# Optimization experiments

Hardware: AMD Instinct MI355X
Metric: run time of the kernel (lower is better)

Reference implementation:

```python
import jax, jax.numpy as jnp
import numpy as np
import math

N, D, C = 1024, 512, 70722
M_MARGIN = 0.4
H_SCALE = 0.333
S_SCALE = 64.0
EPS = 0.001


def setup_inputs() -> dict:
    key = jax.random.key(0)
    k1, k2, k3 = jax.random.split(key, 3)
    x = jax.random.normal(k1, (N, D), dtype=jnp.float32)
    labels = jax.random.randint(k2, (N,), 0, C, dtype=jnp.int64)
    # weights ~ N(0, 0.01) as in nn.Parameter init
    weights = 0.01 * jax.random.normal(k3, (C, D), dtype=jnp.float32)
    return {"x": x, "labels": labels, "weights": weights}


def reference(x, labels, weights):
    # world_size == 1: all-gather is identity and all labels are local.
    x_norms = jnp.maximum(jnp.linalg.norm(x, axis=1, keepdims=True), 1e-8)  # [N,1]

    norm_emb = x / jnp.maximum(jnp.linalg.norm(x, axis=1, keepdims=True), 1e-12)
    norm_w = weights / jnp.maximum(jnp.linalg.norm(weights, axis=1, keepdims=True), 1e-12)
    cosine = jnp.clip(norm_emb @ norm_w.T, -1.0, 1.0)  # [N,C]

    # AdaFace adaptive margin scaler (detached norms; t_alpha=1 -> batch stats = current stats)
    safe_norms = jax.lax.stop_gradient(jnp.clip(x_norms, 0.001, 100.0))  # [N,1]
    batch_mean = jnp.mean(safe_norms)
    batch_std = jnp.std(safe_norms, ddof=1)  # torch .std() is unbiased
    margin_scaler = jnp.clip((safe_norms - batch_mean) / (batch_std + EPS) * H_SCALE, -1.0, 1.0)  # [N,1]

    g_angular = -M_MARGIN * margin_scaler           # [N,1]
    g_add = M_MARGIN + M_MARGIN * margin_scaler     # [N,1]

    onehot = jax.nn.one_hot(labels, C, dtype=cosine.dtype)  # [N,C]

    theta = jnp.arccos(cosine)
    theta_m = jnp.clip(theta + onehot * g_angular, EPS, math.pi - EPS)
    logits = (jnp.cos(theta_m) - onehot * g_add) * S_SCALE  # [N,C]

    logp = jax.nn.log_softmax(logits, axis=-1)
    loss = -jnp.mean(jnp.take_along_axis(logp, labels[:, None], axis=1))
    return loss
```

## Files before the change

kernel.cpp:

```cpp
#include <hip/hip_runtime.h>
#include <hip/hip_bf16.h>
#include <stdint.h>

#define DIM 512
#define NROWS 1024
#define NCLS 70722
#define NCTILE 553

typedef float floatx4 __attribute__((ext_vector_type(4)));

__device__ __forceinline__ unsigned pk4_fp8(float a, float b, float c, float d) {
    unsigned v = 0;
    v = __builtin_amdgcn_cvt_pk_fp8_f32(a, b, v, false);
    v = __builtin_amdgcn_cvt_pk_fp8_f32(c, d, v, true);
    return v;
}

__device__ __forceinline__ float wave_reduce_sum(float s) {
    #pragma unroll
    for (int m = 1; m < 64; m <<= 1) s += __shfl_xor(s, m);
    return s;
}

__global__ __launch_bounds__(256) void prep_kernel(
        const float* __restrict__ x, const float* __restrict__ W,
        const int* __restrict__ labels,
        uint8_t* __restrict__ An, uint8_t* __restrict__ Wn8,
        float* __restrict__ rownorm, float* __restrict__ coslab,
        float* __restrict__ rowsum) {
    int b = blockIdx.x;
    int wv = threadIdx.x >> 6, lane = threadIdx.x & 63;
    if (b < NROWS / 4) {
        if (threadIdx.x < 4) rowsum[b * 4 + threadIdx.x] = 0.0f;
        int row = b * 4 + wv;
        int lab = labels[row];
        const float4* xs = (const float4*)(x + (size_t)row * DIM);
        const float4* ws = (const float4*)(W + (size_t)lab * DIM);
        float4 xa = xs[lane * 2], xb = xs[lane * 2 + 1];
        float4 wa = ws[lane * 2], wb = ws[lane * 2 + 1];
        float dxx = xa.x*xa.x + xa.y*xa.y + xa.z*xa.z + xa.w*xa.w
                  + xb.x*xb.x + xb.y*xb.y + xb.z*xb.z + xb.w*xb.w;
        float dww = wa.x*wa.x + wa.y*wa.y + wa.z*wa.z + wa.w*wa.w
                  + wb.x*wb.x + wb.y*wb.y + wb.z*wb.z + wb.w*wb.w;
        float dxw = xa.x*wa.x + xa.y*wa.y + xa.z*wa.z + xa.w*wa.w
                  + xb.x*wb.x + xb.y*wb.y + xb.z*wb.z + xb.w*wb.w;
        dxx = wave_reduce_sum(dxx);
        dww = wave_reduce_sum(dww);
        dxw = wave_reduce_sum(dxw);
        float norm = sqrtf(dxx);
        float s16 = 16.0f / fmaxf(norm, 1e-12f);
        uint2 p;
        p.x = pk4_fp8(xa.x*s16, xa.y*s16, xa.z*s16, xa.w*s16);
        p.y = pk4_fp8(xb.x*s16, xb.y*s16, xb.z*s16, xb.w*s16);
        *(uint2*)(An + (size_t)row * DIM + lane * 8) = p;
        if (lane == 0) {
            rownorm[row] = norm;
            coslab[row]  = dxw / (fmaxf(norm, 1e-12f) * fmaxf(sqrtf(dww), 1e-12f));
        }
    } else {
        int c = (b - NROWS / 4) * 16 + wv * 4 + (lane >> 4);
        c = min(c, NCLS - 1);
        int l16 = lane & 15;
        const float4* src = (const float4*)(W + (size_t)c * DIM + l16 * 32);
        float4 v[8];
        #pragma unroll
        for (int i = 0; i < 8; ++i) v[i] = src[i];
        float ss = 0.0f;
        #pragma unroll
        for (int i = 0; i < 8; ++i)
            ss += v[i].x*v[i].x + v[i].y*v[i].y + v[i].z*v[i].z + v[i].w*v[i].w;
        ss += __shfl_xor(ss, 1); ss += __shfl_xor(ss, 2);
        ss += __shfl_xor(ss, 4); ss += __shfl_xor(ss, 8);
        float s16 = 16.0f / fmaxf(sqrtf(ss), 1e-12f);
        uint4 q0, q1;
        q0.x = pk4_fp8(v[0].x*s16, v[0].y*s16, v[0].z*s16, v[0].w*s16);
        q0.y = pk4_fp8(v[1].x*s16, v[1].y*s16, v[1].z*s16, v[1].w*s16);
        q0.z = pk4_fp8(v[2].x*s16, v[2].y*s16, v[2].z*s16, v[2].w*s16);
        q0.w = pk4_fp8(v[3].x*s16, v[3].y*s16, v[3].z*s16, v[3].w*s16);
        q1.x = pk4_fp8(v[4].x*s16, v[4].y*s16, v[4].z*s16, v[4].w*s16);
        q1.y = pk4_fp8(v[5].x*s16, v[5].y*s16, v[5].z*s16, v[5].w*s16);
        q1.z = pk4_fp8(v[6].x*s16, v[6].y*s16, v[6].z*s16, v[6].w*s16);
        q1.w = pk4_fp8(v[7].x*s16, v[7].y*s16, v[7].z*s16, v[7].w*s16);
        uint4* dst = (uint4*)(Wn8 + (size_t)c * DIM + l16 * 32);
        dst[0] = q0;
        dst[1] = q1;
    }
}

__global__ __launch_bounds__(256) void gemm5_kernel(
        const uint8_t* __restrict__ An, const uint8_t* __restrict__ Wn8,
        float* __restrict__ rowsum) {
    __shared__ uint8_t As[128 * 64];
    __shared__ uint8_t Bs[128 * 64];
    __shared__ float red[128];
    int b = blockIdx.x;
    int ctile = (b >> 6) * 8 + (b & 7);
    int mtile = (b >> 3) & 7;
    if (ctile >= NCTILE) return;
    int t = threadIdx.x, lane = t & 63, wv = t >> 6;
    if (t < 128) red[t] = 0.0f;

    int sr = lane >> 2;
    int ck = (((lane & 3) ^ (sr & 3)) * 16);
    const uint8_t* aG = An + (size_t)(mtile * 128 + wv * 16 + sr) * DIM + ck;
    int c0 = min(ctile * 128 + wv * 16 + sr,      NCLS - 1);
    int c1 = min(ctile * 128 + 64 + wv * 16 + sr, NCLS - 1);
    const uint8_t* bG0 = Wn8 + (size_t)c0 * DIM + ck;
    const uint8_t* bG1 = Wn8 + (size_t)c1 * DIM + ck;
    uint8_t* aL = As + wv * 16 * 64;
    uint8_t* bL = Bs + wv * 16 * 64;

    int wm = (wv >> 1) * 64, wn = (wv & 1) * 64;
    int fr = lane & 15, fq = lane >> 4;
    int fh = fq >> 1, fl = (fq & 1) * 8;

    floatx4 acc[4][4] = {};

    for (int kc = 0; kc < DIM; kc += 64) {
        __syncthreads();
        __builtin_amdgcn_global_load_lds(
            (const __attribute__((address_space(1))) unsigned int*)(aG + kc),
            (__attribute__((address_space(3))) unsigned int*)(aL), 16, 0, 0);
        __builtin_amdgcn_global_load_lds(
            (const __attribute__((address_space(1))) unsigned int*)(aG + (size_t)64 * DIM + kc),
            (__attribute__((address_space(3))) unsigned int*)(aL + 64 * 64), 16, 0, 0);
        __builtin_amdgcn_global_load_lds(
            (const __attribute__((address_space(1))) unsigned int*)(bG0 + kc),
            (__attribute__((address_space(3))) unsigned int*)(bL), 16, 0, 0);
        __builtin_amdgcn_global_load_lds(
            (const __attribute__((address_space(1))) unsigned int*)(bG1 + kc),
            (__attribute__((address_space(3))) unsigned int*)(bL + 64 * 64), 16, 0, 0);
        __syncthreads();
        long af[2][4], bf[2][4];
        #pragma unroll
        for (int mt = 0; mt < 4; ++mt) {
            int R = wm + mt * 16 + fr;
            const uint8_t* rp = As + R * 64;
            #pragma unroll
            for (int s = 0; s < 2; ++s) {
                int csrc = s * 2 + fh;
                af[s][mt] = *(const long*)(rp + ((csrc ^ (R & 3)) * 16) + fl);
            }
        }
        #pragma unroll
        for (int nt = 0; nt < 4; ++nt) {
            int R = wn + nt * 16 + fr;
            const uint8_t* rp = Bs + R * 64;
            #pragma unroll
            for (int s = 0; s < 2; ++s) {
                int csrc = s * 2 + fh;
                bf[s][nt] = *(const long*)(rp + ((csrc ^ (R & 3)) * 16) + fl);
            }
        }
        #pragma unroll
        for (int s = 0; s < 2; ++s)
            #pragma unroll
            for (int mt = 0; mt < 4; ++mt)
                #pragma unroll
                for (int nt = 0; nt < 4; ++nt)
                    acc[mt][nt] = __builtin_amdgcn_mfma_f32_16x16x32_fp8_fp8(
                        af[s][mt], bf[s][nt], acc[mt][nt], 0, 0, 0);
    }

    const float CLIPC = 0.99999950f;
    const float ISCL  = 1.0f / 256.0f;
    int colbase = ctile * 128 + wn + fr;
    #pragma unroll
    for (int mt = 0; mt < 4; ++mt) {
        #pragma unroll
        for (int reg = 0; reg < 4; ++reg) {
            float s = 0.0f;
            #pragma unroll
            for (int nt = 0; nt < 4; ++nt) {
                int col = colbase + nt * 16;
                float c = acc[mt][nt][reg] * ISCL;
                c = fminf(fmaxf(c, -CLIPC), CLIPC);
                float term = __expf(64.0f * c - 64.0f);
                s += (col < NCLS) ? term : 0.0f;
            }
            s += __shfl_xor(s, 1); s += __shfl_xor(s, 2);
            s += __shfl_xor(s, 4); s += __shfl_xor(s, 8);
            if (fr == 0) atomicAdd(&red[wm + mt * 16 + fq * 4 + reg], s);
        }
    }
    __syncthreads();
    if (t < 128) atomicAdd(rowsum + mtile * 128 + t, red[t]);
}

__global__ __launch_bounds__(1024) void finalize_kernel(
        const float* __restrict__ rowsum, const float* __restrict__ coslab,
        const float* __restrict__ rownorm, float* __restrict__ out) {
    __shared__ float sd[1024];
    int t = threadIdx.x;
    float v = fminf(fmaxf(rownorm[t], 0.001f), 100.0f);
    sd[t] = v; __syncthreads();
    for (int s = 512; s > 0; s >>= 1) { if (t < s) sd[t] += sd[t + s]; __syncthreads(); }
    float mean = sd[0] * (1.0f / 1024.0f);
    __syncthreads();
    float d = v - mean;
    sd[t] = d * d; __syncthreads();
    for (int s = 512; s > 0; s >>= 1) { if (t < s) sd[t] += sd[t + s]; __syncthreads(); }
    float stdv = sqrtf(sd[0] * (1.0f / 1023.0f));
    float ms = d / (stdv + 0.001f) * 0.333f;
    ms = fminf(fmaxf(ms, -1.0f), 1.0f);
    float g_ang = -0.4f * ms;
    float g_add =  0.4f + 0.4f * ms;
    const float CLIPC = 0.99999950f;
    const float PI = 3.14159265358979323846f;
    float cl  = fminf(fmaxf(coslab[t], -1.0f), 1.0f);
    float cne = fminf(fmaxf(cl, -CLIPC), CLIPC);
    float logit_non = 64.0f * cne;
    float theta = acosf(cl);
    float tm = fminf(fmaxf(theta + g_ang, 0.001f), PI - 0.001f);
    float logit_true = (__cosf(tm) - g_add) * 64.0f;
    float ssum = rowsum[t] - __expf(logit_non - 64.0f) + __expf(logit_true - 64.0f);
    float loss = logf(ssum) + 64.0f - logit_true;
    __syncthreads();
    sd[t] = loss; __syncthreads();
    for (int s = 512; s > 0; s >>= 1) { if (t < s) sd[t] += sd[t + s]; __syncthreads(); }
    if (t == 0) out[0] = sd[0] * (1.0f / 1024.0f);
}

extern "C" void kernel_launch(void* const* d_in, const int* in_sizes, int n_in,
                              void* d_out, int out_size, void* d_ws, size_t ws_size,
                              hipStream_t stream) {
    const float* x      = (const float*)d_in[0];
    const int*   labels = (const int*)d_in[1];
    const float* W      = (const float*)d_in[2];
    float* out = (float*)d_out;
    char* ws = (char*)d_ws;

    const size_t SZ_WN8 = 36212736;
    const size_t SZ_AN  = 524288;
    uint8_t* Wn8 = (uint8_t*)ws;
    uint8_t* An  = (uint8_t*)(ws + SZ_WN8);
    float* rownorm = (float*)(ws + SZ_WN8 + SZ_AN);
    float* rowsum  = rownorm + 1024;
    float* coslab  = rowsum + 1024;

    int wblocks = (NCLS + 15) / 16;
    prep_kernel<<<NROWS / 4 + wblocks, 256, 0, stream>>>(
        x, W, labels, An, Wn8, rownorm, coslab, rowsum);
    gemm5_kernel<<<70 * 64, 256, 0, stream>>>(An, Wn8, rowsum);
    finalize_kernel<<<1, 1024, 0, stream>>>(rowsum, coslab, rownorm, out);
}
```

Baseline: 317.1 us.

## Double-buffer LDS tiles in fp8 GEMM and simplify weight quantization mapping

The GEMM now prefetches the next K-chunk into a second LDS buffer with async global-to-LDS loads while computing the current one, using explicit vmcnt waits and barriers instead of two syncthreads per iteration. The LDS swizzle gains an extra XOR term to reduce bank conflicts on fragment reads. The weight prep kernel switches to one wave per class row with full-wave reduction and 8-byte stores, replacing the 16-lanes-per-row layout. This doubles LDS use per block, which may lower occupancy, and the prep change alters memory access granularity.

```diff
diff --git a/kernel.cpp b/kernel.cpp
--- a/kernel.cpp
+++ b/kernel.cpp
@@ -58,40 +58,27 @@
             coslab[row]  = dxw / (fmaxf(norm, 1e-12f) * fmaxf(sqrtf(dww), 1e-12f));
         }
     } else {
-        int c = (b - NROWS / 4) * 16 + wv * 4 + (lane >> 4);
-        c = min(c, NCLS - 1);
-        int l16 = lane & 15;
-        const float4* src = (const float4*)(W + (size_t)c * DIM + l16 * 32);
-        float4 v[8];
-        #pragma unroll
-        for (int i = 0; i < 8; ++i) v[i] = src[i];
-        float ss = 0.0f;
-        #pragma unroll
-        for (int i = 0; i < 8; ++i)
-            ss += v[i].x*v[i].x + v[i].y*v[i].y + v[i].z*v[i].z + v[i].w*v[i].w;
-        ss += __shfl_xor(ss, 1); ss += __shfl_xor(ss, 2);
-        ss += __shfl_xor(ss, 4); ss += __shfl_xor(ss, 8);
-        float s16 = 16.0f / fmaxf(sqrtf(ss), 1e-12f);
-        uint4 q0, q1;
-        q0.x = pk4_fp8(v[0].x*s16, v[0].y*s16, v[0].z*s16, v[0].w*s16);
-        q0.y = pk4_fp8(v[1].x*s16, v[1].y*s16, v[1].z*s16, v[1].w*s16);
-        q0.z = pk4_fp8(v[2].x*s16, v[2].y*s16, v[2].z*s16, v[2].w*s16);
-        q0.w = pk4_fp8(v[3].x*s16, v[3].y*s16, v[3].z*s16, v[3].w*s16);
-        q1.x = pk4_fp8(v[4].x*s16, v[4].y*s16, v[4].z*s16, v[4].w*s16);
-        q1.y = pk4_fp8(v[5].x*s16, v[5].y*s16, v[5].z*s16, v[5].w*s16);
-        q1.z = pk4_fp8(v[6].x*s16, v[6].y*s16, v[6].z*s16, v[6].w*s16);
-        q1.w = pk4_fp8(v[7].x*s16, v[7].y*s16, v[7].z*s16, v[7].w*s16);
-        uint4* dst = (uint4*)(Wn8 + (size_t)c * DIM + l16 * 32);
-        dst[0] = q0;
-        dst[1] = q1;
+        int c = (b - NROWS / 4) * 4 + wv;
+        if (c < NCLS) {
+            const float4* src = (const float4*)(W + (size_t)c * DIM);
+            float4 va = src[lane * 2], vb = src[lane * 2 + 1];
+            float ss = va.x*va.x + va.y*va.y + va.z*va.z + va.w*va.w
+                     + vb.x*vb.x + vb.y*vb.y + vb.z*vb.z + vb.w*vb.w;
+            ss = wave_reduce_sum(ss);
+            float s16 = 16.0f / fmaxf(sqrtf(ss), 1e-12f);
+            uint2 p;
+            p.x = pk4_fp8(va.x*s16, va.y*s16, va.z*s16, va.w*s16);
+            p.y = pk4_fp8(vb.x*s16, vb.y*s16, vb.z*s16, vb.w*s16);
+            *(uint2*)(Wn8 + (size_t)c * DIM + lane * 8) = p;
+        }
     }
 }
 
 __global__ __launch_bounds__(256) void gemm5_kernel(
         const uint8_t* __restrict__ An, const uint8_t* __restrict__ Wn8,
         float* __restrict__ rowsum) {
-    __shared__ uint8_t As[128 * 64];
-    __shared__ uint8_t Bs[128 * 64];
+    __shared__ uint8_t As[2][128 * 64];
+    __shared__ uint8_t Bs[2][128 * 64];
     __shared__ float red[128];
     int b = blockIdx.x;
     int ctile = (b >> 6) * 8 + (b & 7);
@@ -101,14 +88,14 @@
     if (t < 128) red[t] = 0.0f;
 
     int sr = lane >> 2;
-    int ck = (((lane & 3) ^ (sr & 3)) * 16);
+    int gs = (sr & 3) ^ ((sr >> 2) & 3);
+    int ck = (((lane & 3) ^ gs) * 16);
     const uint8_t* aG = An + (size_t)(mtile * 128 + wv * 16 + sr) * DIM + ck;
     int c0 = min(ctile * 128 + wv * 16 + sr,      NCLS - 1);
     int c1 = min(ctile * 128 + 64 + wv * 16 + sr, NCLS - 1);
     const uint8_t* bG0 = Wn8 + (size_t)c0 * DIM + ck;
     const uint8_t* bG1 = Wn8 + (size_t)c1 * DIM + ck;
-    uint8_t* aL = As + wv * 16 * 64;
-    uint8_t* bL = Bs + wv * 16 * 64;
+    int wvoff = wv * 16 * 64;
 
     int wm = (wv >> 1) * 64, wn = (wv & 1) * 64;
     int fr = lane & 15, fq = lane >> 4;
@@ -116,51 +103,62 @@
 
     floatx4 acc[4][4] = {};
 
-    for (int kc = 0; kc < DIM; kc += 64) {
-        __syncthreads();
-        __builtin_amdgcn_global_load_lds(
-            (const __attribute__((address_space(1))) unsigned int*)(aG + kc),
-            (__attribute__((address_space(3))) unsigned int*)(aL), 16, 0, 0);
-        __builtin_amdgcn_global_load_lds(
-            (const __attribute__((address_space(1))) unsigned int*)(aG + (size_t)64 * DIM + kc),
-            (__attribute__((address_space(3))) unsigned int*)(aL + 64 * 64), 16, 0, 0);
-        __builtin_amdgcn_global_load_lds(
-            (const __attribute__((address_space(1))) unsigned int*)(bG0 + kc),
-            (__attribute__((address_space(3))) unsigned int*)(bL), 16, 0, 0);
-        __builtin_amdgcn_global_load_lds(
-            (const __attribute__((address_space(1))) unsigned int*)(bG1 + kc),
-            (__attribute__((address_space(3))) unsigned int*)(bL + 64 * 64), 16, 0, 0);
-        __syncthreads();
-        long af[2][4], bf[2][4];
-        #pragma unroll
-        for (int mt = 0; mt < 4; ++mt) {
-            int R = wm + mt * 16 + fr;
-            const uint8_t* rp = As + R * 64;
-            #pragma unroll
-            for (int s = 0; s < 2; ++s) {
-                int csrc = s * 2 + fh;
-                af[s][mt] = *(const long*)(rp + ((csrc ^ (R & 3)) * 16) + fl);
-            }
-        }
-        #pragma unroll
-        for (int nt = 0; nt < 4; ++nt) {
-            int R = wn + nt * 16 + fr;
-            const uint8_t* rp = Bs + R * 64;
-            #pragma unroll
-            for (int s = 0; s < 2; ++s) {
-                int csrc = s * 2 + fh;
-                bf[s][nt] = *(const long*)(rp + ((csrc ^ (R & 3)) * 16) + fl);
-            }
-        }
-        #pragma unroll
-        for (int s = 0; s < 2; ++s)
-            #pragma unroll
-            for (int mt = 0; mt < 4; ++mt)
-                #pragma unroll
-                for (int nt = 0; nt < 4; ++nt)
-                    acc[mt][nt] = __builtin_amdgcn_mfma_f32_16x16x32_fp8_fp8(
-                        af[s][mt], bf[s][nt], acc[mt][nt], 0, 0, 0);
+#define GLL(gptr, lptr) __builtin_amdgcn_global_load_lds( \
+        (const __attribute__((address_space(1))) unsigned int*)(gptr), \
+        (__attribute__((address_space(3))) unsigned int*)(lptr), 16, 0, 0)
+
+#define STAGE(buf, kc) do { \
+        GLL(aG + (kc),                      As[buf] + wvoff); \
+        GLL(aG + 64 * DIM + (kc),           As[buf] + wvoff + 64 * 64); \
+        GLL(bG0 + (kc),                     Bs[buf] + wvoff); \
+        GLL(bG1 + (kc),                     Bs[buf] + wvoff + 64 * 64); \
+    } while (0)
+
+#define COMPUTE_TILE(Ab, Bb) do { \
+        long af[2][4], bf[2][4]; \
+        _Pragma("unroll") \
+        for (int mt = 0; mt < 4; ++mt) { \
+            int R = wm + mt * 16 + fr; \
+            int gRB = ((R & 3) ^ ((R >> 2) & 3)) * 16; \
+            const uint8_t* rp = (Ab) + R * 64; \
+            af[0][mt] = *(const long*)(rp + ((fh * 16) ^ gRB) + fl); \
+            af[1][mt] = *(const long*)(rp + (((2 + fh) * 16) ^ gRB) + fl); \
+        } \
+        _Pragma("unroll") \
+        for (int nt = 0; nt < 4; ++nt) { \
+            int R = wn + nt * 16 + fr; \
+            int gRB = ((R & 3) ^ ((R >> 2) & 3)) * 16; \
+            const uint8_t* rp = (Bb) + R * 64; \
+            bf[0][nt] = *(const long*)(rp + ((fh * 16) ^ gRB) + fl); \
+            bf[1][nt] = *(const long*)(rp + (((2 + fh) * 16) ^ gRB) + fl); \
+        } \
+        _Pragma("unroll") \
+        for (int s = 0; s < 2; ++s) \
+            _Pragma("unroll") \
+            for (int mt = 0; mt < 4; ++mt) \
+                _Pragma("unroll") \
+                for (int nt = 0; nt < 4; ++nt) \
+                    acc[mt][nt] = __builtin_amdgcn_mfma_f32_16x16x32_fp8_fp8( \
+                        af[s][mt], bf[s][nt], acc[mt][nt], 0, 0, 0); \
+    } while (0)
+
+    STAGE(0, 0);
+    #pragma unroll
+    for (int k = 0; k < 7; ++k) {
+        STAGE((k + 1) & 1, (k + 1) * 64);
+        asm volatile("s_waitcnt vmcnt(4)" ::: "memory");
+        __builtin_amdgcn_s_barrier();
+        COMPUTE_TILE(As[k & 1], Bs[k & 1]);
+        asm volatile("" ::: "memory");
+        __builtin_amdgcn_s_barrier();
     }
+    asm volatile("s_waitcnt vmcnt(0)" ::: "memory");
+    __builtin_amdgcn_s_barrier();
+    COMPUTE_TILE(As[1], Bs[1]);
+
+#undef GLL
+#undef STAGE
+#undef COMPUTE_TILE
 
     const float CLIPC = 0.99999950f;
     const float ISCL  = 1.0f / 256.0f;
@@ -238,7 +236,7 @@
     float* rowsum  = rownorm + 1024;
     float* coslab  = rowsum + 1024;
 
-    int wblocks = (NCLS + 15) / 16;
+    int wblocks = (NCLS + 3) / 4;
     prep_kernel<<<NROWS / 4 + wblocks, 256, 0, stream>>>(
         x, W, labels, An, Wn8, rownorm, coslab, rowsum);
     gemm5_kernel<<<70 * 64, 256, 0, stream>>>(An, Wn8, rowsum);
```

After: 288.1 us. 1.1x faster.
